# Optimization experiments

Hardware: AMD Instinct MI355X
Metric: run time of the kernel (lower is better)

## Reference

```python
import jax, jax.numpy as jnp
import numpy as np

NUM_GRAPHS = 256


def _gcn_norm(edge_index, num_nodes):
    # Add self-loops (PyG GCNConv default) and compute symmetric normalization
    loops = jnp.arange(num_nodes, dtype=edge_index.dtype)
    src = jnp.concatenate([edge_index[0], loops])
    dst = jnp.concatenate([edge_index[1], loops])
    deg = jax.ops.segment_sum(jnp.ones_like(dst, dtype=jnp.float32), dst,
                              num_segments=num_nodes)
    dinv = jnp.where(deg > 0, jax.lax.rsqrt(deg), 0.0)
    norm = dinv[src] * dinv[dst]  # [E + N]
    return src, dst, norm


def _gcn_layer(x, W, b, src, dst, norm, num_nodes):
    h = x @ W                      # transform first (cheaper: N x d_out)
    msg = h[src] * norm[:, None]   # gather + per-edge scale  [E+N, d_out]
    agg = jax.ops.segment_sum(msg, dst, num_segments=num_nodes)
    return agg + b


def setup_inputs() -> dict:
    key = jax.random.key(0)
    ks = jax.random.split(key, 12)
    N, E, F_in = 100000, 1600000, 5
    x = jax.random.normal(ks[0], (N, F_in), dtype=jnp.float32)
    edge_index = jax.random.randint(ks[1], (2, E), 0, N, dtype=jnp.int64)
    batch = jnp.sort(jax.random.randint(ks[2], (N,), 0, NUM_GRAPHS, dtype=jnp.int64))

    def glorot(k, fi, fo):
        s = jnp.sqrt(6.0 / (fi + fo))
        return jax.random.uniform(k, (fi, fo), jnp.float32, -s, s)

    return {
        "x": x, "edge_index": edge_index, "batch": batch,
        "W1": glorot(ks[3], F_in, 64), "b1": jnp.zeros((64,), jnp.float32),
        "W2": glorot(ks[4], 64, 128),  "b2": jnp.zeros((128,), jnp.float32),
        "W3": glorot(ks[5], 128, 64),  "b3": jnp.zeros((64,), jnp.float32),
        "Wfc": glorot(ks[6], 64, 1),   "bfc": jnp.zeros((1,), jnp.float32),
    }


def reference(x, edge_index, batch, W1, b1, W2, b2, W3, b3, Wfc, bfc):
    N = x.shape[0]
    src, dst, norm = _gcn_norm(edge_index, N)
    h = jax.nn.relu(_gcn_layer(x, W1, b1, src, dst, norm, N))
    h = jax.nn.relu(_gcn_layer(h, W2, b2, src, dst, norm, N))
    h = jax.nn.relu(_gcn_layer(h, W3, b3, src, dst, norm, N))
    # global mean pool over graph ids
    sums = jax.ops.segment_sum(h, batch, num_segments=NUM_GRAPHS)
    cnts = jax.ops.segment_sum(jnp.ones((N,), jnp.float32), batch,
                               num_segments=NUM_GRAPHS)
    pooled = sums / jnp.maximum(cnts, 1.0)[:, None]   # [G, 64]
    return jax.nn.sigmoid(pooled @ Wfc + bfc)         # [G, 1]
```

## Files before the change

### kernel.cpp

```cpp
#include <hip/hip_runtime.h>
#include <math.h>

#define NG 256
#define NBK 512
#define BCAP 3584
#define FBN 96

static __device__ __forceinline__ int bucket_lo(int p, int n) {
    return (int)(((long long)p * n + NBK - 1) / NBK);
}

static __device__ __forceinline__ float blo(unsigned u) {
    return __uint_as_float(u << 16);
}
static __device__ __forceinline__ float bhi(unsigned u) {
    return __uint_as_float(u & 0xFFFF0000u);
}
static __device__ __forceinline__ unsigned packbf(float a, float b) {
    unsigned ua = __float_as_uint(a);
    ua = (ua + 0x7FFFu + ((ua >> 16) & 1u)) >> 16;
    unsigned ub = __float_as_uint(b);
    ub = (ub + 0x7FFFu + ((ub >> 16) & 1u)) & 0xFFFF0000u;
    return ua | ub;
}

__global__ void zero_bcur(int* bcur) {
    int i = blockIdx.x * blockDim.x + threadIdx.x;
    if (i < NBK) bcur[i] = i * BCAP;
}

__global__ void bucketA(const int* __restrict__ src, const int* __restrict__ dst,
                        int* bcur, unsigned* stage, int e, int n) {
    __shared__ int cnt[NBK];
    __shared__ int base[NBK];
    int nb = gridDim.x;
    int c0 = (int)((long long)blockIdx.x * e / nb);
    int c1 = (int)((long long)(blockIdx.x + 1) * e / nb);
    for (int k = threadIdx.x; k < NBK; k += blockDim.x) cnt[k] = 0;
    __syncthreads();
    for (int i = c0 + threadIdx.x; i < c1; i += blockDim.x) {
        int d = dst[i];
        int p = (int)((long long)d * NBK / n);
        atomicAdd(&cnt[p], 1);
    }
    __syncthreads();
    for (int k = threadIdx.x; k < NBK; k += blockDim.x)
        base[k] = atomicAdd(&bcur[k], cnt[k]);
    __syncthreads();
    for (int k = threadIdx.x; k < NBK; k += blockDim.x) cnt[k] = 0;
    __syncthreads();
    for (int i = c0 + threadIdx.x; i < c1; i += blockDim.x) {
        int s = src[i], d = dst[i];
        int p = (int)((long long)d * NBK / n);
        int ldst = d - bucket_lo(p, n);
        int lp = atomicAdd(&cnt[p], 1);
        stage[base[p] + lp] = ((unsigned)s << 8) | (unsigned)ldst;
    }
}

__global__ void fillB2(const unsigned* __restrict__ stage,
                       const int* __restrict__ bcur,
                       int* __restrict__ rowptr, float* __restrict__ dinv,
                       int* __restrict__ csrs,
                       const float* __restrict__ x, float* __restrict__ xs,
                       int n, int e) {
    __shared__ int ldeg[256];
    __shared__ int loff[256];
    __shared__ int bstart;
    int p = blockIdx.x;
    int t = threadIdx.x;
    int lo = bucket_lo(p, n), hi = bucket_lo(p + 1, n);
    int nloc = hi - lo;

    {
        int acc = 0;
        for (int k = t; k < p; k += 256) acc += bcur[k] - k * BCAP;
        ldeg[t] = acc;
        __syncthreads();
        for (int off = 128; off > 0; off >>= 1) {
            if (t < off) ldeg[t] += ldeg[t + off];
            __syncthreads();
        }
        if (t == 0) bstart = ldeg[0];
        __syncthreads();
    }

    if (t < 256) ldeg[t] = 0;
    __syncthreads();
    int s0 = p * BCAP, s1 = bcur[p];
    for (int i = s0 + t; i < s1; i += 256)
        atomicAdd(&ldeg[stage[i] & 255u], 1);
    __syncthreads();

    int v = (t < nloc) ? ldeg[t] : 0;
    loff[t] = v;
    __syncthreads();
    for (int off = 1; off < 256; off <<= 1) {
        int u = (t >= off) ? loff[t - off] : 0;
        __syncthreads();
        loff[t] += u;
        __syncthreads();
    }
    if (t < nloc) {
        int start = bstart + loff[t] - v;
        rowptr[lo + t] = start;
        float dv = rsqrtf((float)v + 1.0f);
        dinv[lo + t] = dv;
        const float* xr = x + (size_t)(lo + t) * 5;
        float* xo = xs + (size_t)(lo + t) * 8;
#pragma unroll
        for (int k = 0; k < 5; ++k) xo[k] = xr[k] * dv;
    }
    if (p == NBK - 1 && t == 0) rowptr[n] = e;
    __syncthreads();
    if (t < nloc) ldeg[t] = bstart + loff[t] - v;
    __syncthreads();

    for (int i = s0 + t; i < s1; i += 256) {
        unsigned pk = stage[i];
        int ldst = (int)(pk & 255u);
        int pos = atomicAdd(&ldeg[ldst], 1);
        csrs[pos] = (int)(pk >> 8);
    }
}

__global__ void gather5(const int* __restrict__ rowptr,
                        const int* __restrict__ csrs,
                        const float* __restrict__ dinv,
                        const float* __restrict__ xs,
                        float* __restrict__ z, int n) {
    int i = blockIdx.x * blockDim.x + threadIdx.x;
    if (i >= n) return;
    const float* xr = xs + (size_t)i * 8;
    float4 x4 = *(const float4*)(xr);
    float a0 = x4.x, a1 = x4.y, a2 = x4.z, a3 = x4.w, a4 = xr[4];
    int j = rowptr[i], end = rowptr[i + 1], e1 = end - 1;
    for (; j < end; j += 4) {
        int s[4]; float m[4];
#pragma unroll
        for (int k = 0; k < 4; ++k) {
            int jj = j + k;
            s[k] = csrs[jj <= e1 ? jj : e1];
            m[k] = (jj < end) ? 1.0f : 0.0f;
        }
        float4 r4[4]; float r1[4];
#pragma unroll
        for (int k = 0; k < 4; ++k) {
            const float* r = xs + (size_t)s[k] * 8;
            r4[k] = *(const float4*)(r);
            r1[k] = r[4];
        }
#pragma unroll
        for (int k = 0; k < 4; ++k) {
            a0 = fmaf(m[k], r4[k].x, a0);
            a1 = fmaf(m[k], r4[k].y, a1);
            a2 = fmaf(m[k], r4[k].z, a2);
            a3 = fmaf(m[k], r4[k].w, a3);
            a4 = fmaf(m[k], r1[k], a4);
        }
    }
    float di = dinv[i];
    float* zr = z + (size_t)i * 5;
    zr[0] = a0 * di; zr[1] = a1 * di; zr[2] = a2 * di;
    zr[3] = a3 * di; zr[4] = a4 * di;
}

template<int DOUT, bool BR, bool SCALE, bool OUTBF>
static __device__ __forceinline__ void emit(float o[8], const float* b, int c,
                                            float dsc, void* out, int i) {
    if (BR) {
        float4 b0 = *(const float4*)(b + c * 8);
        float4 b1 = *(const float4*)(b + c * 8 + 4);
        o[0] = fmaxf(o[0] + b0.x, 0.f); o[1] = fmaxf(o[1] + b0.y, 0.f);
        o[2] = fmaxf(o[2] + b0.z, 0.f); o[3] = fmaxf(o[3] + b0.w, 0.f);
        o[4] = fmaxf(o[4] + b1.x, 0.f); o[5] = fmaxf(o[5] + b1.y, 0.f);
        o[6] = fmaxf(o[6] + b1.z, 0.f); o[7] = fmaxf(o[7] + b1.w, 0.f);
    }
    if (SCALE) {
#pragma unroll
        for (int q = 0; q < 8; ++q) o[q] *= dsc;
    }
    if (OUTBF) {
        uint4 pk;
        pk.x = packbf(o[0], o[1]); pk.y = packbf(o[2], o[3]);
        pk.z = packbf(o[4], o[5]); pk.w = packbf(o[6], o[7]);
        *(uint4*)((unsigned*)out + (size_t)i * (DOUT / 2) + c * 4) = pk;
    } else {
        float* op = (float*)out + (size_t)i * DOUT + c * 8;
        float4 o0 = {o[0], o[1], o[2], o[3]};
        float4 o1 = {o[4], o[5], o[6], o[7]};
        *(float4*)(op) = o0;
        *(float4*)(op + 4) = o1;
    }
}

template<int DOUT, bool BR, bool SCALE, bool OUTBF, int NODES>
__global__ void transformB5(const float* __restrict__ xin,
                            const float* __restrict__ W,
                            const float* __restrict__ b,
                            const float* __restrict__ dinv,
                            void* __restrict__ out, int n) {
    const int C = DOUT / 8;
    int tid = blockIdx.x * blockDim.x + threadIdx.x;
    int grp = tid / C;
    int c = tid % C;
    int i0 = grp * NODES;
    if (i0 >= n) return;
    float r[NODES][5];
#pragma unroll
    for (int nn = 0; nn < NODES; ++nn) {
        int idx = i0 + nn < n ? i0 + nn : n - 1;
        const float* row = xin + (size_t)idx * 5;
#pragma unroll
        for (int k = 0; k < 5; ++k) r[nn][k] = row[k];
    }
    float acc[NODES][8];
#pragma unroll
    for (int nn = 0; nn < NODES; ++nn)
#pragma unroll
        for (int q = 0; q < 8; ++q) acc[nn][q] = 0.0f;
#pragma unroll
    for (int k = 0; k < 5; ++k) {
        const float* wp = W + (size_t)k * DOUT + c * 8;
        float4 w0 = *(const float4*)(wp);
        float4 w1 = *(const float4*)(wp + 4);
#pragma unroll
        for (int nn = 0; nn < NODES; ++nn) {
            float v = r[nn][k];
            acc[nn][0] = fmaf(v, w0.x, acc[nn][0]);
            acc[nn][1] = fmaf(v, w0.y, acc[nn][1]);
            acc[nn][2] = fmaf(v, w0.z, acc[nn][2]);
            acc[nn][3] = fmaf(v, w0.w, acc[nn][3]);
            acc[nn][4] = fmaf(v, w1.x, acc[nn][4]);
            acc[nn][5] = fmaf(v, w1.y, acc[nn][5]);
            acc[nn][6] = fmaf(v, w1.z, acc[nn][6]);
            acc[nn][7] = fmaf(v, w1.w, acc[nn][7]);
        }
    }
#pragma unroll
    for (int nn = 0; nn < NODES; ++nn) {
        if (i0 + nn >= n) break;
        float dsc = SCALE ? dinv[i0 + nn] : 1.0f;
        emit<DOUT, BR, SCALE, OUTBF>(acc[nn], b, c, dsc, out, i0 + nn);
    }
}

#define ACCA(AA, V) \
    AA[0] += blo(V.x); AA[1] += bhi(V.x); AA[2] += blo(V.y); AA[3] += bhi(V.y); \
    AA[4] += blo(V.z); AA[5] += bhi(V.z); AA[6] += blo(V.w); AA[7] += bhi(V.w);
#define ACCM(AA, V, M) \
    AA[0] = fmaf(M, blo(V.x), AA[0]); AA[1] = fmaf(M, bhi(V.x), AA[1]); \
    AA[2] = fmaf(M, blo(V.y), AA[2]); AA[3] = fmaf(M, bhi(V.y), AA[3]); \
    AA[4] = fmaf(M, blo(V.z), AA[4]); AA[5] = fmaf(M, bhi(V.z), AA[5]); \
    AA[6] = fmaf(M, blo(V.w), AA[6]); AA[7] = fmaf(M, bhi(V.w), AA[7]);

static __device__ __forceinline__ void gather_row(const int* __restrict__ rowptr,
                                                  const int* __restrict__ csrs,
                                                  const unsigned* __restrict__ g,
                                                  int i, int c, float o[8]) {
    uint4 sv = *(const uint4*)(g + (size_t)i * 32 + c * 4);
    float a0[8], a1[8], a2[8], a3[8];
    a0[0] = blo(sv.x); a0[1] = bhi(sv.x); a0[2] = blo(sv.y); a0[3] = bhi(sv.y);
    a0[4] = blo(sv.z); a0[5] = bhi(sv.z); a0[6] = blo(sv.w); a0[7] = bhi(sv.w);
#pragma unroll
    for (int q = 0; q < 8; ++q) { a1[q] = 0.0f; a2[q] = 0.0f; a3[q] = 0.0f; }
    int j = rowptr[i], end = rowptr[i + 1];
    for (; j + 8 <= end; j += 8) {
        uint4 v0 = *(const uint4*)(g + (size_t)csrs[j]     * 32 + c * 4);
        uint4 v1 = *(const uint4*)(g + (size_t)csrs[j + 1] * 32 + c * 4);
        uint4 v2 = *(const uint4*)(g + (size_t)csrs[j + 2] * 32 + c * 4);
        uint4 v3 = *(const uint4*)(g + (size_t)csrs[j + 3] * 32 + c * 4);
        uint4 v4 = *(const uint4*)(g + (size_t)csrs[j + 4] * 32 + c * 4);
        uint4 v5 = *(const uint4*)(g + (size_t)csrs[j + 5] * 32 + c * 4);
        uint4 v6 = *(const uint4*)(g + (size_t)csrs[j + 6] * 32 + c * 4);
        uint4 v7 = *(const uint4*)(g + (size_t)csrs[j + 7] * 32 + c * 4);
        ACCA(a0, v0); ACCA(a1, v1); ACCA(a2, v2); ACCA(a3, v3);
        ACCA(a0, v4); ACCA(a1, v5); ACCA(a2, v6); ACCA(a3, v7);
    }
    if (j < end) {
        int e1 = end - 1;
        int sx[8]; float mm[8];
#pragma unroll
        for (int k = 0; k < 8; ++k) {
            int jj = j + k;
            sx[k] = csrs[jj <= e1 ? jj : e1];
            mm[k] = (jj < end) ? 1.0f : 0.0f;
        }
        uint4 v0 = *(const uint4*)(g + (size_t)sx[0] * 32 + c * 4);
        uint4 v1 = *(const uint4*)(g + (size_t)sx[1] * 32 + c * 4);
        uint4 v2 = *(const uint4*)(g + (size_t)sx[2] * 32 + c * 4);
        uint4 v3 = *(const uint4*)(g + (size_t)sx[3] * 32 + c * 4);
        uint4 v4 = *(const uint4*)(g + (size_t)sx[4] * 32 + c * 4);
        uint4 v5 = *(const uint4*)(g + (size_t)sx[5] * 32 + c * 4);
        uint4 v6 = *(const uint4*)(g + (size_t)sx[6] * 32 + c * 4);
        uint4 v7 = *(const uint4*)(g + (size_t)sx[7] * 32 + c * 4);
        ACCM(a0, v0, mm[0]); ACCM(a1, v1, mm[1]);
        ACCM(a2, v2, mm[2]); ACCM(a3, v3, mm[3]);
        ACCM(a0, v4, mm[4]); ACCM(a1, v5, mm[5]);
        ACCM(a2, v6, mm[6]); ACCM(a3, v7, mm[7]);
    }
#pragma unroll
    for (int q = 0; q < 8; ++q) o[q] = (a0[q] + a1[q]) + (a2[q] + a3[q]);
}

template<bool BR>
__global__ void gatherBF(const int* __restrict__ rowptr,
                         const int* __restrict__ csrs,
                         const float* __restrict__ dinv,
                         const float* __restrict__ b,
                         const unsigned* __restrict__ g,
                         float* __restrict__ z, int n) {
    int tid = blockIdx.x * blockDim.x + threadIdx.x;
    int i = tid >> 3;
    int c = tid & 7;
    if (i >= n) return;
    float o[8];
    gather_row(rowptr, csrs, g, i, c, o);
    float di = dinv[i];
#pragma unroll
    for (int q = 0; q < 8; ++q) o[q] *= di;
    if (BR) {
        float4 b0 = *(const float4*)(b + c * 8);
        float4 b1 = *(const float4*)(b + c * 8 + 4);
        o[0] = fmaxf(o[0] + b0.x, 0.f); o[1] = fmaxf(o[1] + b0.y, 0.f);
        o[2] = fmaxf(o[2] + b0.z, 0.f); o[3] = fmaxf(o[3] + b0.w, 0.f);
        o[4] = fmaxf(o[4] + b1.x, 0.f); o[5] = fmaxf(o[5] + b1.y, 0.f);
        o[6] = fmaxf(o[6] + b1.z, 0.f); o[7] = fmaxf(o[7] + b1.w, 0.f);
    }
    float* zp = z + (size_t)i * 64 + c * 8;
    float4 z0 = {o[0], o[1], o[2], o[3]};
    float4 z1 = {o[4], o[5], o[6], o[7]};
    *(float4*)(zp) = z0;
    *(float4*)(zp + 4) = z1;
}

__global__ void layer23(const int* __restrict__ rowptr,
                        const int* __restrict__ csrs,
                        const float* __restrict__ dinv,
                        const float* __restrict__ b2v,
                        const unsigned* __restrict__ g,
                        const float* __restrict__ W2,
                        const float* __restrict__ W3,
                        unsigned* __restrict__ t3, int n) {
    __shared__ unsigned z2s[FBN][36];
    __shared__ unsigned h2s[FBN][68];
    int t = threadIdx.x;
    int base = blockIdx.x * FBN;

    {
        int nd = t >> 3, c = t & 7;
        for (int pass = 0; pass < 3; ++pass) {
            int lr = pass * 32 + nd;
            int i = base + lr;
            if (i < n) {
                float o[8];
                gather_row(rowptr, csrs, g, i, c, o);
                float di = dinv[i];
                uint4 pk;
                pk.x = packbf(o[0] * di, o[1] * di);
                pk.y = packbf(o[2] * di, o[3] * di);
                pk.z = packbf(o[4] * di, o[5] * di);
                pk.w = packbf(o[6] * di, o[7] * di);
                *(uint4*)&z2s[lr][c * 4] = pk;
            }
        }
    }
    __syncthreads();

    {
        int c2 = t & 15;
        int ng = t >> 4;
        float acc[6][8];
#pragma unroll
        for (int nn = 0; nn < 6; ++nn)
#pragma unroll
            for (int q = 0; q < 8; ++q) acc[nn][q] = 0.0f;
        for (int k0 = 0; k0 < 64; k0 += 8) {
            uint4 r[6];
#pragma unroll
            for (int nn = 0; nn < 6; ++nn)
                r[nn] = *(const uint4*)&z2s[ng + 16 * nn][k0 >> 1];
#pragma unroll
            for (int kk = 0; kk < 8; ++kk) {
                const float* wp = W2 + (size_t)(k0 + kk) * 128 + c2 * 8;
                float4 w0 = *(const float4*)(wp);
                float4 w1 = *(const float4*)(wp + 4);
#pragma unroll
                for (int nn = 0; nn < 6; ++nn) {
                    unsigned u = (&r[nn].x)[kk >> 1];
                    float v = (kk & 1) ? bhi(u) : blo(u);
                    acc[nn][0] = fmaf(v, w0.x, acc[nn][0]);
                    acc[nn][1] = fmaf(v, w0.y, acc[nn][1]);
                    acc[nn][2] = fmaf(v, w0.z, acc[nn][2]);
                    acc[nn][3] = fmaf(v, w0.w, acc[nn][3]);
                    acc[nn][4] = fmaf(v, w1.x, acc[nn][4]);
                    acc[nn][5] = fmaf(v, w1.y, acc[nn][5]);
                    acc[nn][6] = fmaf(v, w1.z, acc[nn][6]);
                    acc[nn][7] = fmaf(v, w1.w, acc[nn][7]);
                }
            }
        }
        float4 b0 = *(const float4*)(b2v + c2 * 8);
        float4 b1 = *(const float4*)(b2v + c2 * 8 + 4);
#pragma unroll
        for (int nn = 0; nn < 6; ++nn) {
            float o[8];
            o[0] = fmaxf(acc[nn][0] + b0.x, 0.f);
            o[1] = fmaxf(acc[nn][1] + b0.y, 0.f);
            o[2] = fmaxf(acc[nn][2] + b0.z, 0.f);
            o[3] = fmaxf(acc[nn][3] + b0.w, 0.f);
            o[4] = fmaxf(acc[nn][4] + b1.x, 0.f);
            o[5] = fmaxf(acc[nn][5] + b1.y, 0.f);
            o[6] = fmaxf(acc[nn][6] + b1.z, 0.f);
            o[7] = fmaxf(acc[nn][7] + b1.w, 0.f);
            uint4 pk;
            pk.x = packbf(o[0], o[1]); pk.y = packbf(o[2], o[3]);
            pk.z = packbf(o[4], o[5]); pk.w = packbf(o[6], o[7]);
            *(uint4*)&h2s[ng + 16 * nn][c2 * 4] = pk;
        }
    }
    __syncthreads();

    {
        int c3 = t & 7;
        int ng = t >> 3;
        float acc[3][8];
#pragma unroll
        for (int nn = 0; nn < 3; ++nn)
#pragma unroll
            for (int q = 0; q < 8; ++q) acc[nn][q] = 0.0f;
        for (int k0 = 0; k0 < 128; k0 += 8) {
            uint4 r[3];
#pragma unroll
            for (int nn = 0; nn < 3; ++nn)
                r[nn] = *(const uint4*)&h2s[ng + 32 * nn][k0 >> 1];
#pragma unroll
            for (int kk = 0; kk < 8; ++kk) {
                const float* wp = W3 + (size_t)(k0 + kk) * 64 + c3 * 8;
                float4 w0 = *(const float4*)(wp);
                float4 w1 = *(const float4*)(wp + 4);
#pragma unroll
                for (int nn = 0; nn < 3; ++nn) {
                    unsigned u = (&r[nn].x)[kk >> 1];
                    float v = (kk & 1) ? bhi(u) : blo(u);
                    acc[nn][0] = fmaf(v, w0.x, acc[nn][0]);
                    acc[nn][1] = fmaf(v, w0.y, acc[nn][1]);
                    acc[nn][2] = fmaf(v, w0.z, acc[nn][2]);
                    acc[nn][3] = fmaf(v, w0.w, acc[nn][3]);
                    acc[nn][4] = fmaf(v, w1.x, acc[nn][4]);
                    acc[nn][5] = fmaf(v, w1.y, acc[nn][5]);
                    acc[nn][6] = fmaf(v, w1.z, acc[nn][6]);
                    acc[nn][7] = fmaf(v, w1.w, acc[nn][7]);
                }
            }
        }
#pragma unroll
        for (int nn = 0; nn < 3; ++nn) {
            int i = base + ng + 32 * nn;
            if (i < n) {
                float ds = dinv[i];
                uint4 pk;
                pk.x = packbf(acc[nn][0] * ds, acc[nn][1] * ds);
                pk.y = packbf(acc[nn][2] * ds, acc[nn][3] * ds);
                pk.z = packbf(acc[nn][4] * ds, acc[nn][5] * ds);
                pk.w = packbf(acc[nn][6] * ds, acc[nn][7] * ds);
                *(uint4*)(t3 + (size_t)i * 32 + c3 * 4) = pk;
            }
        }
    }
}

__global__ void pool(const float* __restrict__ h3, const int* __restrict__ batch,
                     const float* __restrict__ Wfc, const float* __restrict__ bfc,
                     float* __restrict__ out, int n) {
    int g = blockIdx.x;
    int lane = threadIdx.x & 63;
    int w = threadIdx.x >> 6;
    int lo = 0, hi = n;
    while (lo < hi) { int m = (lo + hi) >> 1; if (batch[m] < g) lo = m + 1; else hi = m; }
    int start = lo;
    hi = n;
    while (lo < hi) { int m = (lo + hi) >> 1; if (batch[m] < g + 1) lo = m + 1; else hi = m; }
    int end = lo;
    float a0 = 0.f, a1 = 0.f, a2 = 0.f, a3 = 0.f;
    int m = start + w;
    for (; m + 12 < end; m += 16) {
        a0 += h3[(size_t)m * 64 + lane];
        a1 += h3[(size_t)(m + 4) * 64 + lane];
        a2 += h3[(size_t)(m + 8) * 64 + lane];
        a3 += h3[(size_t)(m + 12) * 64 + lane];
    }
    for (; m < end; m += 4) a0 += h3[(size_t)m * 64 + lane];
    __shared__ float sh[4][64];
    sh[w][lane] = (a0 + a1) + (a2 + a3);
    __syncthreads();
    if (w == 0) {
        float v = (sh[0][lane] + sh[1][lane]) + (sh[2][lane] + sh[3][lane]);
        float cnt = (float)(end - start);
        v = (v / fmaxf(cnt, 1.0f)) * Wfc[lane];
#pragma unroll
        for (int off = 32; off > 0; off >>= 1) v += __shfl_down(v, off, 64);
        if (lane == 0) out[g] = 1.0f / (1.0f + expf(-(v + bfc[0])));
    }
}

static inline int cdiv(long long a, int b) { return (int)((a + b - 1) / b); }

extern "C" void kernel_launch(void* const* d_in, const int* in_sizes, int n_in,
                              void* d_out, int out_size, void* d_ws, size_t ws_size,
                              hipStream_t stream) {
    const float* x   = (const float*)d_in[0];
    const int*   ei  = (const int*)d_in[1];
    const int*   bat = (const int*)d_in[2];
    const float* W1  = (const float*)d_in[3];
    const float* b1  = (const float*)d_in[4];
    const float* W2  = (const float*)d_in[5];
    const float* b2  = (const float*)d_in[6];
    const float* W3  = (const float*)d_in[7];
    const float* b3  = (const float*)d_in[8];
    const float* Wfc = (const float*)d_in[9];
    const float* bfc = (const float*)d_in[10];
    float* out = (float*)d_out;

    const int N = in_sizes[0] / 5;
    const int E = in_sizes[1] / 2;
    const int* src = ei;
    const int* ds  = ei + E;

    char* wsb = (char*)d_ws;
    size_t off = 0;
#define A256(X) (((X) + (size_t)255) & ~(size_t)255)
    float* dinv   = (float*)(wsb + off); off = A256(off + (size_t)N * 4);
    int*   rowptr = (int*)(wsb + off);   off = A256(off + (size_t)(N + 4) * 4);
    int*   bcur   = (int*)(wsb + off);   off = A256(off + (size_t)NBK * 4);
    int*   csrs   = (int*)(wsb + off);   off = A256(off + (size_t)E * 4);
    float* A      = (float*)(wsb + off); off = A256(off + (size_t)N * 128 * 4);
    float* B      = (float*)(wsb + off);
#undef A256
    unsigned* stage = (unsigned*)A;
    float*    xs    = A + (size_t)(1 << 21);
    float*    z1    = A;
    unsigned* h1bf  = (unsigned*)B;
    unsigned* t3bf  = (unsigned*)A;
    float*    h3    = B;

    const int Blk = 256;

    zero_bcur<<<2, 256, 0, stream>>>(bcur);
    bucketA<<<256, 256, 0, stream>>>(src, ds, bcur, stage, E, N);
    fillB2<<<NBK, 256, 0, stream>>>(stage, bcur, rowptr, dinv, csrs, x, xs, N, E);

    gather5<<<cdiv(N, Blk), Blk, 0, stream>>>(rowptr, csrs, dinv, xs, z1, N);
    transformB5<64, true, true, true, 2>
        <<<cdiv((long long)cdiv(N, 2) * 8, Blk), Blk, 0, stream>>>(
        z1, W1, b1, dinv, h1bf, N);

    layer23<<<cdiv(N, FBN), 256, 0, stream>>>(
        rowptr, csrs, dinv, b2, h1bf, W2, W3, t3bf, N);

    gatherBF<true><<<cdiv((long long)N * 8, Blk), Blk, 0, stream>>>(
        rowptr, csrs, dinv, b3, t3bf, h3, N);

    pool<<<NG, 256, 0, stream>>>(h3, bat, Wfc, bfc, out, N);
}
```

Before: 293.5 us.

## Split fused layer-2 gather+transform into separate gather and transform kernels

Splits the fused layer23 kernel, which gathered neighbor rows into shared memory and then ran the W2/W3 transform, into two kernels. A standalone gatherBF pass now writes the aggregated layer-2 features to global memory as bf16, and a new transform23 kernel reads them directly. The point is to give the irregular gather its own launch with full thread-level parallelism (8 threads per node across the grid), instead of 3 serial passes per block followed by a barrier. The cost is an extra global write and read of a bf16 buffer of N×64 values, plus one more launch.

```diff
diff --git a/kernel.cpp b/kernel.cpp
--- a/kernel.cpp
+++ b/kernel.cpp
@@ -303,13 +303,13 @@
     for (int q = 0; q < 8; ++q) o[q] = (a0[q] + a1[q]) + (a2[q] + a3[q]);
 }
 
-template<bool BR>
+template<bool BR, bool OUTBF>
 __global__ void gatherBF(const int* __restrict__ rowptr,
                          const int* __restrict__ csrs,
                          const float* __restrict__ dinv,
                          const float* __restrict__ b,
                          const unsigned* __restrict__ g,
-                         float* __restrict__ z, int n) {
+                         void* __restrict__ z, int n) {
     int tid = blockIdx.x * blockDim.x + threadIdx.x;
     int i = tid >> 3;
     int c = tid & 7;
@@ -327,49 +327,39 @@
         o[4] = fmaxf(o[4] + b1.x, 0.f); o[5] = fmaxf(o[5] + b1.y, 0.f);
         o[6] = fmaxf(o[6] + b1.z, 0.f); o[7] = fmaxf(o[7] + b1.w, 0.f);
     }
-    float* zp = z + (size_t)i * 64 + c * 8;
-    float4 z0 = {o[0], o[1], o[2], o[3]};
-    float4 z1 = {o[4], o[5], o[6], o[7]};
-    *(float4*)(zp) = z0;
-    *(float4*)(zp + 4) = z1;
-}
-
-__global__ void layer23(const int* __restrict__ rowptr,
-                        const int* __restrict__ csrs,
-                        const float* __restrict__ dinv,
-                        const float* __restrict__ b2v,
-                        const unsigned* __restrict__ g,
-                        const float* __restrict__ W2,
-                        const float* __restrict__ W3,
-                        unsigned* __restrict__ t3, int n) {
-    __shared__ unsigned z2s[FBN][36];
+    if (OUTBF) {
+        uint4 pk;
+        pk.x = packbf(o[0], o[1]); pk.y = packbf(o[2], o[3]);
+        pk.z = packbf(o[4], o[5]); pk.w = packbf(o[6], o[7]);
+        *(uint4*)((unsigned*)z + (size_t)i * 32 + c * 4) = pk;
+    } else {
+        float* zp = (float*)z + (size_t)i * 64 + c * 8;
+        float4 z0 = {o[0], o[1], o[2], o[3]};
+        float4 z1 = {o[4], o[5], o[6], o[7]};
+        *(float4*)(zp) = z0;
+        *(float4*)(zp + 4) = z1;
+    }
+}
+
+__global__ void transform23(const unsigned* __restrict__ z2,
+                            const float* __restrict__ b2v,
+                            const float* __restrict__ W2,
+                            const float* __restrict__ W3,
+                            const float* __restrict__ dinv,
+                            unsigned* __restrict__ t3, int n) {
     __shared__ unsigned h2s[FBN][68];
     int t = threadIdx.x;
     int base = blockIdx.x * FBN;
 
     {
-        int nd = t >> 3, c = t & 7;
-        for (int pass = 0; pass < 3; ++pass) {
-            int lr = pass * 32 + nd;
-            int i = base + lr;
-            if (i < n) {
-                float o[8];
-                gather_row(rowptr, csrs, g, i, c, o);
-                float di = dinv[i];
-                uint4 pk;
-                pk.x = packbf(o[0] * di, o[1] * di);
-                pk.y = packbf(o[2] * di, o[3] * di);
-                pk.z = packbf(o[4] * di, o[5] * di);
-                pk.w = packbf(o[6] * di, o[7] * di);
-                *(uint4*)&z2s[lr][c * 4] = pk;
-            }
-        }
-    }
-    __syncthreads();
-
-    {
         int c2 = t & 15;
         int ng = t >> 4;
+        int idx[6];
+#pragma unroll
+        for (int nn = 0; nn < 6; ++nn) {
+            int i = base + ng + 16 * nn;
+            idx[nn] = i < n ? i : n - 1;
+        }
         float acc[6][8];
 #pragma unroll
         for (int nn = 0; nn < 6; ++nn)
@@ -379,7 +369,7 @@
             uint4 r[6];
 #pragma unroll
             for (int nn = 0; nn < 6; ++nn)
-                r[nn] = *(const uint4*)&z2s[ng + 16 * nn][k0 >> 1];
+                r[nn] = *(const uint4*)(z2 + (size_t)idx[nn] * 32 + (k0 >> 1));
 #pragma unroll
             for (int kk = 0; kk < 8; ++kk) {
                 const float* wp = W2 + (size_t)(k0 + kk) * 128 + c2 * 8;
@@ -542,6 +532,7 @@
     float*    z1    = A;
     unsigned* h1bf  = (unsigned*)B;
     unsigned* t3bf  = (unsigned*)A;
+    unsigned* z2bf  = (unsigned*)A + (size_t)(1 << 22);
     float*    h3    = B;
 
     const int Blk = 256;
@@ -555,10 +546,12 @@
         <<<cdiv((long long)cdiv(N, 2) * 8, Blk), Blk, 0, stream>>>(
         z1, W1, b1, dinv, h1bf, N);
 
-    layer23<<<cdiv(N, FBN), 256, 0, stream>>>(
-        rowptr, csrs, dinv, b2, h1bf, W2, W3, t3bf, N);
-
-    gatherBF<true><<<cdiv((long long)N * 8, Blk), Blk, 0, stream>>>(
+    gatherBF<false, true><<<cdiv((long long)N * 8, Blk), Blk, 0, stream>>>(
+        rowptr, csrs, dinv, nullptr, h1bf, z2bf, N);
+    transform23<<<cdiv(N, FBN), 256, 0, stream>>>(
+        z2bf, b2, W2, W3, dinv, t3bf, N);
+
+    gatherBF<true, false><<<cdiv((long long)N * 8, Blk), Blk, 0, stream>>>(
         rowptr, csrs, dinv, b3, t3bf, h3, N);
 
     pool<<<NG, 256, 0, stream>>>(h3, bat, Wfc, bfc, out, N);
```

Measured after the change: 313.4 us. 1.07x slower.
